# Kernel tuning notes

Hardware: AMD Instinct MI355X
Metric: run time of the kernel (lower is better)

The kernel has to match this reference:

```python
import jax, jax.numpy as jnp
import numpy as np

DIM = 4096
N_HEADS = 32
N_KV_HEADS = 8
HEAD_DIM = DIM // N_HEADS  # 128
N_REP = N_HEADS // N_KV_HEADS  # 4
BSZ = 2
SEQ = 2048
ROPE_THETA = 500000.0


def setup_inputs() -> dict:
    key = jax.random.key(0)
    ks = jax.random.split(key, 10)
    x = jax.random.normal(ks[0], (BSZ, SEQ, DIM), dtype=jnp.float32)
    # RoPE frequencies (Llama style): theta^{-2i/d}, angles = pos * freq
    inv_freq = 1.0 / (ROPE_THETA ** (jnp.arange(0, HEAD_DIM, 2, dtype=jnp.float32) / HEAD_DIM))  # [64]
    angles = jnp.arange(SEQ, dtype=jnp.float32)[:, None] * inv_freq[None, :]  # [SEQ, 64]
    freqs_cos = jnp.cos(angles)
    freqs_sin = jnp.sin(angles)
    # causal additive mask for prefill
    mask = jnp.triu(jnp.full((SEQ, SEQ), -jnp.inf, dtype=jnp.float32), k=1)
    scale = 0.02
    wq = jax.random.normal(ks[1], (DIM, DIM), dtype=jnp.float32) * scale
    bq = jnp.zeros((DIM,), dtype=jnp.float32)
    wk = jax.random.normal(ks[2], (N_KV_HEADS * HEAD_DIM, DIM), dtype=jnp.float32) * scale
    bk = jnp.zeros((N_KV_HEADS * HEAD_DIM,), dtype=jnp.float32)
    wv = jax.random.normal(ks[3], (N_KV_HEADS * HEAD_DIM, DIM), dtype=jnp.float32) * scale
    bv = jnp.zeros((N_KV_HEADS * HEAD_DIM,), dtype=jnp.float32)
    wo = jax.random.normal(ks[4], (DIM, DIM), dtype=jnp.float32) * scale
    bo = jnp.zeros((DIM,), dtype=jnp.float32)
    return {"x": x, "freqs_cos": freqs_cos, "freqs_sin": freqs_sin, "mask": mask,
            "wq": wq, "bq": bq, "wk": wk, "bk": bk, "wv": wv, "bv": bv, "wo": wo, "bo": bo}


def _apply_rope(t, cos, sin):
    # t: [b, s, h, d]; cos/sin: [s, d//2]; pairs are consecutive (view_as_complex)
    a = t[..., 0::2]
    b = t[..., 1::2]
    cos = cos[None, :, None, :]
    sin = sin[None, :, None, :]
    out_a = a * cos - b * sin
    out_b = a * sin + b * cos
    return jnp.stack([out_a, out_b], axis=-1).reshape(t.shape)


def reference(x, freqs_cos, freqs_sin, mask, wq, bq, wk, bk, wv, bv, wo, bo):
    bsz, seq_len, _ = x.shape
    xq = (x @ wq.T + bq).reshape(bsz, seq_len, N_HEADS, HEAD_DIM)
    xk = (x @ wk.T + bk).reshape(bsz, seq_len, N_KV_HEADS, HEAD_DIM)
    xv = (x @ wv.T + bv).reshape(bsz, seq_len, N_KV_HEADS, HEAD_DIM)
    xq = _apply_rope(xq, freqs_cos, freqs_sin)
    xk = _apply_rope(xk, freqs_cos, freqs_sin)
    # start_pos=0 prefill: cache write then slice [:, :seq_len] returns xk/xv
    keys, values = xk, xv
    # repeat_kv via GQA grouping inside einsum (equivalent to materialized expand)
    # q: [b, s, kvh, rep, d]
    q = xq.reshape(bsz, seq_len, N_KV_HEADS, N_REP, HEAD_DIM)
    scores = jnp.einsum('bqgrd,bkgd->bgrqk', q, keys) / jnp.sqrt(jnp.float32(HEAD_DIM))
    scores = scores + mask[None, None, None, :, :]
    probs = jax.nn.softmax(scores.astype(jnp.float32), axis=-1).astype(xq.dtype)
    out = jnp.einsum('bgrqk,bkgd->bqgrd', probs, values)
    out = out.reshape(bsz, seq_len, DIM)
    return out @ wo.T + bo
```

## Files before the change

kernel.cpp:

```cpp
#include <hip/hip_runtime.h>


using bf16x8 = __attribute__((ext_vector_type(8))) short;
using f32x4  = __attribute__((ext_vector_type(4))) float;
using u16x4  = __attribute__((ext_vector_type(4))) unsigned short;
using u16x8  = __attribute__((ext_vector_type(8))) unsigned short;

__device__ __forceinline__ float bf2f(unsigned short h) {
    unsigned int u = ((unsigned int)h) << 16;
    return __builtin_bit_cast(float, u);
}
__device__ __forceinline__ unsigned short f2bf(float f) {
    unsigned int u = __builtin_bit_cast(unsigned int, f);
    u += 0x7FFFu + ((u >> 16) & 1u);
    return (unsigned short)(u >> 16);
}
__device__ __forceinline__ f32x4 mfma16(bf16x8 a, bf16x8 b, f32x4 c) {
    return __builtin_amdgcn_mfma_f32_16x16x32_bf16(a, b, c, 0, 0, 0);
}

#define GLOAD_LDS16(gp, lp)                                                   \
    __builtin_amdgcn_global_load_lds(                                         \
        (const __attribute__((address_space(1))) void*)(gp),                  \
        (__attribute__((address_space(3))) void*)(lp), 16, 0, 0)

__global__ __launch_bounds__(256) void cvt_kernel(
    const float* __restrict__ src, unsigned short* __restrict__ dst, int n)
{
    const int i = (blockIdx.x * 256 + threadIdx.x) * 8;
    if (i >= n) return;
    float4 a = *(const float4*)(src + i);
    float4 b = *(const float4*)(src + i + 4);
    u16x8 o;
    o[0] = f2bf(a.x); o[1] = f2bf(a.y); o[2] = f2bf(a.z); o[3] = f2bf(a.w);
    o[4] = f2bf(b.x); o[5] = f2bf(b.y); o[6] = f2bf(b.z); o[7] = f2bf(b.w);
    *(u16x8*)(dst + i) = o;
}

template<int MODE>
__global__ __launch_bounds__(256) void gemm_bias(
    const unsigned short* __restrict__ A, const unsigned short* __restrict__ W,
    const float* __restrict__ bias, const float* __restrict__ bias2,
    void* __restrict__ Cv, void* __restrict__ Cv2,
    int M, int N, int K)
{
    __shared__ __align__(16) unsigned short As[2][128 * 32];
    __shared__ __align__(16) unsigned short Bs[2][128 * 32];

    const int tid  = threadIdx.x;
    const int lane = tid & 63;
    const int wv   = tid >> 6;
    const int ln   = lane & 15, quad = lane >> 4;
    const int wr   = wv >> 1, wc = wv & 1;
    const int m0 = blockIdx.y * 128 + wr * 64;
    const int n0 = blockIdx.x * 128 + wc * 64;

    const int srow = tid >> 2;
    const int scol = (tid & 3) * 8;
    const unsigned short* aptr = A + (size_t)(blockIdx.y * 128 + srow) * K + scol;
    const unsigned short* bptr = W + (size_t)(blockIdx.x * 128 + srow) * K + scol;
    const size_t rowskip = (size_t)64 * K;

#define GEMM_STAGE(c)                                                         \
    do {                                                                      \
        GLOAD_LDS16(aptr,           &As[c][tid * 8]);                         \
        GLOAD_LDS16(aptr + rowskip, &As[c][2048 + tid * 8]);                  \
        GLOAD_LDS16(bptr,           &Bs[c][tid * 8]);                         \
        GLOAD_LDS16(bptr + rowskip, &Bs[c][2048 + tid * 8]);                  \
        aptr += 32; bptr += 32;                                               \
    } while (0)

    f32x4 acc[4][4];
#pragma unroll
    for (int i = 0; i < 4; ++i)
#pragma unroll
        for (int j = 0; j < 4; ++j) acc[i][j] = f32x4{0.f, 0.f, 0.f, 0.f};

    GEMM_STAGE(0);
    __syncthreads();

    const int nk = K >> 5;
    int cur = 0;
    for (int kt = 0; kt < nk; ++kt) {
        if (kt + 1 < nk) GEMM_STAGE(cur ^ 1);

        bf16x8 af[4], bfr[4];
#pragma unroll
        for (int i = 0; i < 4; ++i)
            af[i]  = *(const bf16x8*)(&As[cur][(wr * 64 + i * 16 + ln) * 32 + quad * 8]);
#pragma unroll
        for (int j = 0; j < 4; ++j)
            bfr[j] = *(const bf16x8*)(&Bs[cur][(wc * 64 + j * 16 + ln) * 32 + quad * 8]);
#pragma unroll
        for (int i = 0; i < 4; ++i)
#pragma unroll
            for (int j = 0; j < 4; ++j)
                acc[i][j] = mfma16(af[i], bfr[j], acc[i][j]);

        __syncthreads();
        cur ^= 1;
    }
#undef GEMM_STAGE

#pragma unroll
    for (int j = 0; j < 4; ++j) {
        const int col = n0 + j * 16 + ln;
        const float bval = (MODE == 1 && col >= 1024) ? bias2[col - 1024] : bias[col];
#pragma unroll
        for (int i = 0; i < 4; ++i) {
            const int rowb = m0 + i * 16 + quad * 4;
            if (MODE == 2) {
                float* C = (float*)Cv;
#pragma unroll
                for (int r = 0; r < 4; ++r)
                    C[(size_t)(rowb + r) * N + col] = acc[i][j][r] + bval;
            } else if (MODE == 0) {
                unsigned short* C = (unsigned short*)Cv;
#pragma unroll
                for (int r = 0; r < 4; ++r)
                    C[(size_t)(rowb + r) * N + col] = f2bf(acc[i][j][r] + bval);
            } else {
                if (col < 1024) {
                    unsigned short* C = (unsigned short*)Cv;
#pragma unroll
                    for (int r = 0; r < 4; ++r)
                        C[(size_t)(rowb + r) * 1024 + col] = f2bf(acc[i][j][r] + bval);
                } else {
                    unsigned short* C = (unsigned short*)Cv2;
                    const int vcol = col - 1024;
                    const int gg = vcol >> 7, d = vcol & 127;
                    const int bb = rowb >> 11, s = rowb & 2047;
                    u16x4 pk;
#pragma unroll
                    for (int r = 0; r < 4; ++r) pk[r] = f2bf(acc[i][j][r] + bval);
                    *(u16x4*)(C + (((size_t)(bb * 8 + gg) * 128 + d) * 2048 + s)) = pk;
                }
            }
        }
    }
}

__global__ __launch_bounds__(256) void rope_kernel(
    unsigned short* __restrict__ Q, unsigned short* __restrict__ Kb,
    const float* __restrict__ fc, const float* __restrict__ fs)
{
    const int idx = blockIdx.x * 256 + threadIdx.x;
    const int NQP = 2 * 2048 * 32 * 64;
    const int NKP = 2 * 2048 * 8 * 64;
    unsigned short* t; int s, i; float scale;
    if (idx < NQP) {
        i = idx & 63; const int bsh = idx >> 6;
        s = (bsh >> 5) & 2047;
        t = Q + ((size_t)bsh << 7) + 2 * i;
        scale = 0.12751743f;
    } else {
        const int p = idx - NQP;
        if (p >= NKP) return;
        i = p & 63; const int bsh = p >> 6;
        s = (bsh >> 3) & 2047;
        t = Kb + ((size_t)bsh << 7) + 2 * i;
        scale = 1.0f;
    }
    const float c = fc[s * 64 + i], sn = fs[s * 64 + i];
    const unsigned int u = *(const unsigned int*)t;
    const float a = bf2f((unsigned short)(u & 0xffff));
    const float b = bf2f((unsigned short)(u >> 16));
    const unsigned int lo = f2bf((a * c - b * sn) * scale);
    const unsigned int hi = f2bf((a * sn + b * c) * scale);
    *(unsigned int*)t = lo | (hi << 16);
}

__global__ __launch_bounds__(512, 4) void attn_kernel(
    const unsigned short* __restrict__ Q, const unsigned short* __restrict__ K,
    const unsigned short* __restrict__ Vt, unsigned short* __restrict__ O)
{
    __shared__ __align__(16) unsigned short Ks[2][32 * 128];
    __shared__ __align__(16) unsigned short Vs[2][128 * 32];
    __shared__ __align__(16) unsigned short p_s[8][16][40];

    const int tid  = threadIdx.x;
    const int lane = tid & 63;
    const int wv   = tid >> 6;
    const int ln = lane & 15, quad = lane >> 4;
    const int bx = blockIdx.x;
    const int g = bx & 7, b = (bx >> 3) & 1;
    const int pairIdx = bx >> 4;
    const int h = wv >> 1;
    const int rh = (wv & 1) * 16;

    const int krow = tid >> 4, kcs = (tid & 15) ^ (krow & 7);
    const int vrow = tid >> 2, vcs = (tid & 3) ^ (vrow & 3);
    const unsigned short* ksrc0 =
        K + ((size_t)(b * 2048 + krow) * 8 + g) * 128 + kcs * 8;
    const unsigned short* vsrc0 =
        Vt + (size_t)(b * 8 + g) * 262144 + (size_t)vrow * 2048 + vcs * 8;

#define ATTN_STAGE(c)                                                         \
    do {                                                                      \
        GLOAD_LDS16(ksrc, &Ks[c][tid * 8]);                                   \
        GLOAD_LDS16(vsrc, &Vs[c][tid * 8]);                                   \
        ksrc += 32768; vsrc += 32;                                            \
    } while (0)

#pragma unroll
    for (int ph = 0; ph < 2; ++ph) {
        const int j   = ph ? (63 - pairIdx) : pairIdx;
        const int q0w = j * 32 + rh;
        const int nk  = j + 1;

        bf16x8 qf[4];
        {
            const unsigned short* qrow =
                Q + ((size_t)((b * 2048 + q0w + ln) * 32 + g * 4 + h)) * 128 + quad * 8;
#pragma unroll
            for (int d4 = 0; d4 < 4; ++d4) qf[d4] = *(const bf16x8*)(qrow + d4 * 32);
        }

        f32x4 oacc[8];
#pragma unroll
        for (int t = 0; t < 8; ++t) oacc[t] = f32x4{0.f, 0.f, 0.f, 0.f};
        float li[4] = {0.f, 0.f, 0.f, 0.f};

        const unsigned short* ksrc = ksrc0;
        const unsigned short* vsrc = vsrc0;

        ATTN_STAGE(0);
        __syncthreads();

        for (int kt = 0; kt < nk; ++kt) {
            const int cur = kt & 1;
            const int k0  = kt * 32;
            if (kt + 1 < nk) ATTN_STAGE(cur ^ 1);

            const bool edge = (kt == nk - 1);
            const unsigned short* Kc = Ks[cur];
            const unsigned short* Vc = Vs[cur];

            bf16x8 kf0[4], kf1[4];
#pragma unroll
            for (int d4 = 0; d4 < 4; ++d4) {
                const int isw = ((d4 * 4 + quad) ^ (ln & 7)) * 8;
                kf0[d4] = *(const bf16x8*)(Kc + ln * 128 + isw);
                kf1[d4] = *(const bf16x8*)(Kc + (16 + ln) * 128 + isw);
            }
            f32x4 s0 = f32x4{0.f, 0.f, 0.f, 0.f};
            f32x4 s1 = f32x4{0.f, 0.f, 0.f, 0.f};
#pragma unroll
            for (int d4 = 0; d4 < 4; ++d4) s0 = mfma16(qf[d4], kf0[d4], s0);
#pragma unroll
            for (int d4 = 0; d4 < 4; ++d4) s1 = mfma16(qf[d4], kf1[d4], s1);
#pragma unroll
            for (int r = 0; r < 4; ++r) {
                float e0 = __builtin_amdgcn_exp2f(s0[r]);
                float e1 = __builtin_amdgcn_exp2f(s1[r]);
                if (edge) {
                    const int qg = q0w + quad * 4 + r;
                    e0 = (k0 + ln <= qg)      ? e0 : 0.f;
                    e1 = (k0 + 16 + ln <= qg) ? e1 : 0.f;
                }
                li[r] += e0 + e1;
                p_s[wv][quad * 4 + r][ln]      = f2bf(e0);
                p_s[wv][quad * 4 + r][16 + ln] = f2bf(e1);
            }
            __asm__ volatile("s_waitcnt lgkmcnt(0)" ::: "memory");
            bf16x8 pf = *(const bf16x8*)(&p_s[wv][ln][quad * 8]);
            const int vsw = (quad ^ (ln & 3)) * 8;
#pragma unroll
            for (int t = 0; t < 8; ++t) {
                bf16x8 vf = *(const bf16x8*)(Vc + (t * 16 + ln) * 32 + vsw);
                oacc[t] = mfma16(pf, vf, oacc[t]);
            }
            __syncthreads();
        }

        float inv[4];
#pragma unroll
        for (int r = 0; r < 4; ++r) {
            float l = li[r];
#pragma unroll
            for (int off = 1; off < 16; off <<= 1) l += __shfl_xor(l, off);
            inv[r] = 1.0f / l;
        }
        unsigned short* ob =
            O + ((size_t)((b * 2048 + q0w + quad * 4) * 32 + g * 4 + h)) * 128;
#pragma unroll
        for (int t = 0; t < 8; ++t)
#pragma unroll
            for (int r = 0; r < 4; ++r)
                ob[(size_t)r * 4096 + t * 16 + ln] = f2bf(oacc[t][r] * inv[r]);
    }
#undef ATTN_STAGE
}

extern "C" void kernel_launch(void* const* d_in, const int* in_sizes, int n_in,
                              void* d_out, int out_size, void* d_ws, size_t ws_size,
                              hipStream_t stream)
{
    const float* x  = (const float*)d_in[0];
    const float* fc = (const float*)d_in[1];
    const float* fs = (const float*)d_in[2];
    const float* wq = (const float*)d_in[4];
    const float* bq = (const float*)d_in[5];
    const float* wk = (const float*)d_in[6];
    const float* bk = (const float*)d_in[7];
    const float* wv = (const float*)d_in[8];
    const float* bv = (const float*)d_in[9];
    const float* wo = (const float*)d_in[10];
    const float* bo = (const float*)d_in[11];

    unsigned short* wsp = (unsigned short*)d_ws;
    unsigned short* xb  = wsp;
    unsigned short* wqb = xb  + 16777216;
    unsigned short* wkb = wqb + 16777216;
    unsigned short* wvb = wkb + 4194304;
    unsigned short* Qb  = wvb + 4194304;
    unsigned short* Kb  = Qb  + 16777216;
    unsigned short* Vt  = Kb  + 4194304;

    cvt_kernel<<<8192, 256, 0, stream>>>(x,  xb,  16777216);
    cvt_kernel<<<8192, 256, 0, stream>>>(wq, wqb, 16777216);
    cvt_kernel<<<2048, 256, 0, stream>>>(wk, wkb, 4194304);
    cvt_kernel<<<2048, 256, 0, stream>>>(wv, wvb, 4194304);

    gemm_bias<0><<<dim3(32, 32), 256, 0, stream>>>(xb, wqb, bq, nullptr,
                                                   Qb, nullptr, 4096, 4096, 4096);
    gemm_bias<1><<<dim3(16, 32), 256, 0, stream>>>(xb, wkb, bk, bv,
                                                   Kb, Vt, 4096, 2048, 4096);

    cvt_kernel<<<8192, 256, 0, stream>>>(wo, wqb, 16777216);

    rope_kernel<<<40960, 256, 0, stream>>>(Qb, Kb, fc, fs);
    attn_kernel<<<512, 512, 0, stream>>>(Qb, Kb, Vt, xb);

    gemm_bias<2><<<dim3(32, 32), 256, 0, stream>>>(xb, wqb, bo, nullptr,
                                                   d_out, nullptr, 4096, 4096, 4096);
}
```

Measured before the change: 825.9 us.

## Use 256x256-tile triple-buffered GEMM for Q and output projections

After: 789.4 us. 4.4% less time.

```diff
diff --git a/kernel.cpp b/kernel.cpp
--- a/kernel.cpp
+++ b/kernel.cpp
@@ -38,6 +38,110 @@
 }
 
 template<int MODE>
+__global__ __launch_bounds__(512, 2) void gemm256(
+    const unsigned short* __restrict__ A, const unsigned short* __restrict__ W,
+    const float* __restrict__ bias, void* __restrict__ Cv,
+    int M, int N, int K)
+{
+    __shared__ __align__(16) unsigned short As[3][256 * 32];
+    __shared__ __align__(16) unsigned short Bs[3][256 * 32];
+
+    const int nwg  = gridDim.x * gridDim.y;
+    const int bid0 = blockIdx.y * gridDim.x + blockIdx.x;
+    const int bid  = (bid0 & 7) * (nwg >> 3) + (bid0 >> 3);
+    const int bx = bid % gridDim.x, by = bid / gridDim.x;
+
+    const int tid  = threadIdx.x;
+    const int lane = tid & 63;
+    const int wid  = tid >> 6;
+    const int ln = lane & 15, quad = lane >> 4;
+    const int wr = wid >> 2, wc = wid & 3;
+    const int m0 = by * 256, n0 = bx * 256;
+
+    const int srow = tid >> 2;
+    const int scol = (tid & 3) * 8;
+    const unsigned short* aptr = A + (size_t)(m0 + srow) * K + scol;
+    const unsigned short* bptr = W + (size_t)(n0 + srow) * K + scol;
+    const size_t rowskip = (size_t)128 * K;
+
+#define G256_STAGE(ab, bb)                                                    \
+    do {                                                                      \
+        GLOAD_LDS16(aptr,           (ab) + tid * 8);                          \
+        GLOAD_LDS16(aptr + rowskip, (ab) + 4096 + tid * 8);                   \
+        GLOAD_LDS16(bptr,           (bb) + tid * 8);                          \
+        GLOAD_LDS16(bptr + rowskip, (bb) + 4096 + tid * 8);                   \
+        aptr += 32; bptr += 32;                                               \
+    } while (0)
+
+    f32x4 acc[8][4];
+#pragma unroll
+    for (int i = 0; i < 8; ++i)
+#pragma unroll
+        for (int j = 0; j < 4; ++j) acc[i][j] = f32x4{0.f, 0.f, 0.f, 0.f};
+
+    unsigned short *a0 = As[0], *a1 = As[1], *a2 = As[2];
+    unsigned short *b0 = Bs[0], *b1 = Bs[1], *b2 = Bs[2];
+
+    const int nk = K >> 5;
+    G256_STAGE(a0, b0);
+    G256_STAGE(a1, b1);
+    asm volatile("s_waitcnt vmcnt(4)" ::: "memory");
+    __builtin_amdgcn_s_barrier();
+
+    const int aoff = (wr * 128 + ln) * 32 + quad * 8;
+    const int boff = (wc * 64 + ln) * 32 + quad * 8;
+
+    for (int kt = 0; kt < nk; ++kt) {
+        const bool more = (kt + 2 < nk);
+        if (more) G256_STAGE(a2, b2);
+
+        bf16x8 af[8], bfr[4];
+#pragma unroll
+        for (int i = 0; i < 8; ++i) af[i]  = *(const bf16x8*)(a0 + aoff + i * 512);
+#pragma unroll
+        for (int j = 0; j < 4; ++j) bfr[j] = *(const bf16x8*)(b0 + boff + j * 512);
+
+        __builtin_amdgcn_s_setprio(1);
+#pragma unroll
+        for (int i = 0; i < 8; ++i)
+#pragma unroll
+            for (int j = 0; j < 4; ++j)
+                acc[i][j] = mfma16(af[i], bfr[j], acc[i][j]);
+        __builtin_amdgcn_s_setprio(0);
+
+        if (more) asm volatile("s_waitcnt vmcnt(4) lgkmcnt(0)" ::: "memory");
+        else      asm volatile("s_waitcnt vmcnt(0) lgkmcnt(0)" ::: "memory");
+        __builtin_amdgcn_s_barrier();
+
+        unsigned short* t;
+        t = a0; a0 = a1; a1 = a2; a2 = t;
+        t = b0; b0 = b1; b1 = b2; b2 = t;
+    }
+#undef G256_STAGE
+
+#pragma unroll
+    for (int j = 0; j < 4; ++j) {
+        const int col = n0 + wc * 64 + j * 16 + ln;
+        const float bval = bias[col];
+#pragma unroll
+        for (int i = 0; i < 8; ++i) {
+            const int rowb = m0 + wr * 128 + i * 16 + quad * 4;
+            if (MODE == 2) {
+                float* C = (float*)Cv;
+#pragma unroll
+                for (int r = 0; r < 4; ++r)
+                    C[(size_t)(rowb + r) * N + col] = acc[i][j][r] + bval;
+            } else {
+                unsigned short* C = (unsigned short*)Cv;
+#pragma unroll
+                for (int r = 0; r < 4; ++r)
+                    C[(size_t)(rowb + r) * N + col] = f2bf(acc[i][j][r] + bval);
+            }
+        }
+    }
+}
+
+template<int MODE>
 __global__ __launch_bounds__(256) void gemm_bias(
     const unsigned short* __restrict__ A, const unsigned short* __restrict__ W,
     const float* __restrict__ bias, const float* __restrict__ bias2,
@@ -109,12 +213,7 @@
 #pragma unroll
         for (int i = 0; i < 4; ++i) {
             const int rowb = m0 + i * 16 + quad * 4;
-            if (MODE == 2) {
-                float* C = (float*)Cv;
-#pragma unroll
-                for (int r = 0; r < 4; ++r)
-                    C[(size_t)(rowb + r) * N + col] = acc[i][j][r] + bval;
-            } else if (MODE == 0) {
+            if (MODE == 0) {
                 unsigned short* C = (unsigned short*)Cv;
 #pragma unroll
                 for (int r = 0; r < 4; ++r)
@@ -322,8 +421,7 @@
     cvt_kernel<<<2048, 256, 0, stream>>>(wk, wkb, 4194304);
     cvt_kernel<<<2048, 256, 0, stream>>>(wv, wvb, 4194304);
 
-    gemm_bias<0><<<dim3(32, 32), 256, 0, stream>>>(xb, wqb, bq, nullptr,
-                                                   Qb, nullptr, 4096, 4096, 4096);
+    gemm256<0><<<dim3(16, 16), 512, 0, stream>>>(xb, wqb, bq, Qb, 4096, 4096, 4096);
     gemm_bias<1><<<dim3(16, 32), 256, 0, stream>>>(xb, wkb, bk, bv,
                                                    Kb, Vt, 4096, 2048, 4096);
 
@@ -332,6 +430,6 @@
     rope_kernel<<<40960, 256, 0, stream>>>(Qb, Kb, fc, fs);
     attn_kernel<<<512, 512, 0, stream>>>(Qb, Kb, Vt, xb);
 
-    gemm_bias<2><<<dim3(32, 32), 256, 0, stream>>>(xb, wqb, bo, nullptr,
-                                                   d_out, nullptr, 4096, 4096, 4096);
-}
+    gemm256<2><<<dim3(16, 16), 512, 0, stream>>>(xb, wqb, bo,
+                                                 d_out, 4096, 4096, 4096);
+}
```
